# Kernel optimization log

Hardware: AMD Instinct MI355X
Metric: run time of the kernel (lower is better)

The kernel has to match this reference:

```python
import jax, jax.numpy as jnp
import numpy as np

B = 1024          # batch
D = 6             # data_dim
H = 128           # hidden_dim
VW = 256          # vf_hidden_dim (MLP width and output)
LS = 22           # logsig_dim (first entry dropped in vector field)
NI = 64           # number of log-signature intervals
NSTEPS = 64       # fixed Heun steps over [0, 1]


def setup_inputs() -> dict:
    key = jax.random.key(0)
    ks = jax.random.split(key, 12)
    ts = jnp.linspace(0.0, 1.0, NI + 1, dtype=jnp.float32)
    logsig = 0.1 * jax.random.normal(ks[0], (B, NI, LS), dtype=jnp.float32)
    x0 = jax.random.normal(ks[1], (B, D), dtype=jnp.float32)
    def lin(k, out_d, in_d):
        s = 1.0 / np.sqrt(in_d)
        kw, kb = jax.random.split(k)
        W = jax.random.uniform(kw, (out_d, in_d), jnp.float32, -s, s)
        b = jax.random.uniform(kb, (out_d,), jnp.float32, -s, s)
        return W, b
    W_vf1, b_vf1 = lin(ks[2], VW, H)    # VectorField MLP: hidden -> width
    W_vf2, b_vf2 = lin(ks[3], VW, VW)   # width -> vf out, final tanh
    Wm, bm = lin(ks[4], H * (LS - 1), VW)  # mlp_linear
    W1, b1 = lin(ks[5], H, D)           # linear1
    W2, b2 = lin(ks[6], 10, H)          # linear2 (label_dim=10)
    return {"ts": ts, "logsig": logsig, "x0": x0,
            "W_vf1": W_vf1, "b_vf1": b_vf1, "W_vf2": W_vf2, "b_vf2": b_vf2,
            "Wm": Wm, "bm": bm, "W1": W1, "b1": b1, "W2": W2, "b2": b2}


def reference(ts, logsig, x0, W_vf1, b_vf1, W_vf2, b_vf2, Wm, bm, W1, b1, W2, b2):
    intervals = ts                      # breakpoints, shape (NI+1,)
    dt = (ts[-1] - ts[0]) / NSTEPS
    ls_tail = logsig[:, :, 1:]          # (B, NI, LS-1), drop leading logsig term

    def vf(y):                          # VectorField MLP, batched: (B,H)->(B,VW)
        h = jax.nn.relu(jnp.einsum("bh,wh->bw", y, W_vf1) + b_vf1)
        return jnp.tanh(jnp.einsum("bw,vw->bv", h, W_vf2) + b_vf2)

    def func(t, y):                     # dy/dt, shape (B, H)
        idx = jnp.clip(jnp.searchsorted(intervals, t), 1, NI)
        A = (jnp.einsum("bv,ov->bo", vf(y), Wm) + bm).reshape(-1, H, LS - 1)
        ls = ls_tail[:, idx - 1]        # (B, LS-1)
        width = intervals[idx] - intervals[idx - 1]
        return jnp.einsum("bhl,bl->bh", A, ls) / width

    def heun_step(y, t):
        k1 = func(t, y)
        k2 = func(t + dt, y + dt * k1)
        return y + 0.5 * dt * (k1 + k2), None

    y0 = jnp.einsum("bd,hd->bh", x0, W1) + b1
    step_ts = ts[0] + dt * jnp.arange(NSTEPS, dtype=jnp.float32)
    yT, _ = jax.lax.scan(heun_step, y0, step_ts)
    return jax.nn.softmax(jnp.einsum("bh,ch->bc", yT, W2) + b2, axis=-1)
```

## Files before the change

### kernel.cpp

```cpp
#include <hip/hip_runtime.h>
#include <hip/hip_bf16.h>

typedef float f32x4 __attribute__((ext_vector_type(4)));
typedef int   i32x4 __attribute__((ext_vector_type(4)));
typedef short s16x8 __attribute__((ext_vector_type(8)));
typedef unsigned short u16;

#define NGP 32
#define BT 16
#define NWG 256
#define NTH 512
#define PREPTH 256
#define H 128
#define VW 256
#define NI 64
#define NSTEPS 64

#define OFF_FRAG16 0
#define OFF_WMQ    196608
#define OFF_BMF    884736
#define OFF_SCF    895488
#define OFF_SINV   896000
#define OFF_YBUF   896512
#define YBUF_BYTES 1048576

#define MFMA_BF16(a,b,c) __builtin_amdgcn_mfma_f32_16x16x32_bf16(a,b,c,0,0,0)
#define MFMA_I8(a,b,c)   __builtin_amdgcn_mfma_i32_16x16x64_i8(a,b,c,0,0,0)

__device__ __forceinline__ u16 bf16u(float f) {
  union { float f; unsigned u; } x; x.f = f;
  return (u16)((x.u + 0x7fffu + ((x.u >> 16) & 1u)) >> 16);
}
__device__ __forceinline__ float b2f(u16 u) {
  union { unsigned u; float f; } x; x.u = ((unsigned)u) << 16;
  return x.f;
}

__global__ void prep_scales(const float* __restrict__ Wm, char* __restrict__ ws) {
  __shared__ float red[4];
  const int tid = threadIdx.x;
  const int h = blockIdx.x;
  float m = 0.f;
  for (int i = tid; i < 21 * VW; i += PREPTH) m = fmaxf(m, fabsf(Wm[h * 21 * VW + i]));
  for (int off = 32; off > 0; off >>= 1) m = fmaxf(m, __shfl_down(m, off));
  if ((tid & 63) == 0) red[tid >> 6] = m;
  __syncthreads();
  if (tid == 0) {
    m = fmaxf(fmaxf(red[0], red[1]), fmaxf(red[2], red[3]));
    m = fmaxf(m, 1e-20f);
    ((float*)(ws + OFF_SCF))[h]  = m / 16129.f;
    ((float*)(ws + OFF_SINV))[h] = 127.f / m;
  }
}

__global__ void prep_pack(const float* __restrict__ Wvf1, const float* __restrict__ Wvf2,
                          const float* __restrict__ Wm, const float* __restrict__ bmv,
                          char* __restrict__ ws) {
  int idx = blockIdx.x * blockDim.x + threadIdx.x;
  if (idx < 98304) {
    u16* w16 = (u16*)(ws + OFF_FRAG16);
    float val;
    if (idx < 32768) {
      int e = idx;
      int j = e & 7, ln = (e >> 3) & 63, nt = (e >> 9) & 15, kk = e >> 13;
      val = Wvf1[(nt * 16 + (ln & 15)) * H + kk * 32 + (ln >> 4) * 8 + j];
    } else {
      int e = idx - 32768;
      int j = e & 7, ln = (e >> 3) & 63, nt = (e >> 9) & 15, kk = e >> 13;
      val = Wvf2[(nt * 16 + (ln & 15)) * VW + kk * 32 + (ln >> 4) * 8 + j];
    }
    w16[idx] = bf16u(val);
  } else if (idx < 98304 + 688128) {
    int b = idx - 98304;
    int j = b & 15, lane = (b >> 4) & 63, kk = (b >> 10) & 3, rem = b >> 12;
    int l = rem % 21, nt = rem / 21;
    int h = nt * 16 + (lane & 15);
    int w = kk * 64 + (lane >> 4) * 16 + j;
    float sinv = ((const float*)(ws + OFF_SINV))[h];
    float val = Wm[(size_t)(h * 21 + l) * VW + w];
    int q = (int)lrintf(val * sinv);
    q = min(127, max(-127, q));
    ((signed char*)(ws + OFF_WMQ))[b] = (signed char)q;
  } else if (idx < 98304 + 688128 + 2688) {
    int b = idx - (98304 + 688128);
    int hh = b & 15, rem = b >> 4;
    int l = rem % 21, nt = rem / 21;
    ((float*)(ws + OFF_BMF))[b] = bmv[(nt * 16 + hh) * 21 + l];
  }
}

__global__ __launch_bounds__(NTH, 1) void rde_main(
    const float* __restrict__ logsig, const float* __restrict__ x0,
    const float* __restrict__ W1, const float* __restrict__ b1,
    const float* __restrict__ bvf1, const float* __restrict__ bvf2,
    const float* __restrict__ W2, const float* __restrict__ b2,
    char* __restrict__ ws, float* __restrict__ out) {
  __shared__ __align__(16) signed char WmL[86016];
  __shared__ __align__(16) u16   YB [2][BT][H + 8];
  __shared__ __align__(16) u16   V1R[BT][VW + 8];
  __shared__ __align__(16) signed char V2QH[4096];
  __shared__ __align__(16) float LSF[2][2][21][BT];
  __shared__ __align__(16) float part[8][BT][17];
  __shared__ __align__(16) float bmL[336];
  __shared__ float scL[16];
  __shared__ float LG[32][10];

  const int tid = threadIdx.x;
  const int lane = tid & 63;
  const int wv = tid >> 6;
  const int c = lane & 15;
  const int kg = lane >> 4;
  const int bid = blockIdx.x;
  const int Gp = (bid & 7) * 4 + (bid >> 6);
  const int t = (bid >> 3) & 7;
  const int b0 = Gp * 32;
  unsigned* __restrict__ ybuf = (unsigned*)(ws + OFF_YBUF);
  const s16x8* __restrict__ fr16 = (const s16x8*)(ws + OFF_FRAG16);
  const f32x4 zf = {0.f, 0.f, 0.f, 0.f};
  const i32x4 zi = {0, 0, 0, 0};

  s16x8 w1r[2][4], w2r[2][8];
#pragma unroll
  for (int n = 0; n < 2; ++n) {
#pragma unroll
    for (int kk = 0; kk < 4; ++kk) w1r[n][kk] = fr16[(kk * 16 + wv * 2 + n) * 64 + lane];
#pragma unroll
    for (int kk = 0; kk < 8; ++kk) w2r[n][kk] = fr16[4096 + (kk * 16 + wv * 2 + n) * 64 + lane];
  }
  float bv1[2], bv2[2];
#pragma unroll
  for (int n = 0; n < 2; ++n) {
    bv1[n] = bvf1[wv * 32 + n * 16 + c];
    bv2[n] = bvf2[wv * 32 + n * 16 + c];
  }

  {
    const i32x4* wsrc = (const i32x4*)(ws + OFF_WMQ + t * 86016);
    i32x4* wdst = (i32x4*)WmL;
    for (int e = tid; e < 5376; e += NTH) wdst[e] = wsrc[e];
  }
  if (tid < 16) scL[tid] = ((const float*)(ws + OFF_SCF))[t * 16 + tid];
  for (int e = tid; e < 336; e += NTH) bmL[e] = ((const float*)(ws + OFF_BMF))[t * 336 + e];

  for (int e = tid; e < 2 * BT * H; e += NTH) {
    int tt = e >> 11, r = (e >> 7) & 15, h = e & 127;
    float a = b1[h];
#pragma unroll
    for (int d = 0; d < 6; ++d) a += x0[(b0 + tt * 16 + r) * 6 + d] * W1[h * 6 + d];
    YB[tt][r][h] = bf16u(a);
  }
  float y0s = 0.f, y1s = 0.f, yp0s = 0.f, yp1s = 0.f;
  if (tid < 256) {
    int r = tid >> 4, hh = tid & 15, h = t * 16 + hh;
    float a0 = b1[h], a1 = b1[h];
#pragma unroll
    for (int d = 0; d < 6; ++d) {
      a0 += x0[(b0 + r) * 6 + d] * W1[h * 6 + d];
      a1 += x0[(b0 + 16 + r) * 6 + d] * W1[h * 6 + d];
    }
    y0s = a0; y1s = a1;
  }

  auto STAGE = [&](int T, int iv) {
    for (int e = tid; e < BT * 21; e += NTH) {
      int r = e / 21, l = e - r * 21;
      LSF[T][iv & 1][l][r] = logsig[((size_t)(b0 + T * 16 + r) * NI + iv) * 22 + 1 + l];
    }
  };
  auto S1 = [&](int T) {
    s16x8 ay0 = *(const s16x8*)&YB[T][c][0 * 32 + kg * 8];
    s16x8 ay1 = *(const s16x8*)&YB[T][c][1 * 32 + kg * 8];
    s16x8 ay2 = *(const s16x8*)&YB[T][c][2 * 32 + kg * 8];
    s16x8 ay3 = *(const s16x8*)&YB[T][c][3 * 32 + kg * 8];
    f32x4 pA = MFMA_BF16(ay0, w1r[0][0], zf), pB = MFMA_BF16(ay0, w1r[1][0], zf);
    pA = MFMA_BF16(ay1, w1r[0][1], pA);  pB = MFMA_BF16(ay1, w1r[1][1], pB);
    pA = MFMA_BF16(ay2, w1r[0][2], pA);  pB = MFMA_BF16(ay2, w1r[1][2], pB);
    pA = MFMA_BF16(ay3, w1r[0][3], pA);  pB = MFMA_BF16(ay3, w1r[1][3], pB);
#pragma unroll
    for (int q = 0; q < 4; ++q) {
      V1R[kg * 4 + q][wv * 32 + c]      = bf16u(fmaxf(pA[q] + bv1[0], 0.f));
      V1R[kg * 4 + q][wv * 32 + 16 + c] = bf16u(fmaxf(pB[q] + bv1[1], 0.f));
    }
  };
  auto S2 = [&]() {
    s16x8 av0 = *(const s16x8*)&V1R[c][0 * 32 + kg * 8];
    s16x8 av1 = *(const s16x8*)&V1R[c][1 * 32 + kg * 8];
    s16x8 av2 = *(const s16x8*)&V1R[c][2 * 32 + kg * 8];
    s16x8 av3 = *(const s16x8*)&V1R[c][3 * 32 + kg * 8];
    s16x8 av4 = *(const s16x8*)&V1R[c][4 * 32 + kg * 8];
    s16x8 av5 = *(const s16x8*)&V1R[c][5 * 32 + kg * 8];
    s16x8 av6 = *(const s16x8*)&V1R[c][6 * 32 + kg * 8];
    s16x8 av7 = *(const s16x8*)&V1R[c][7 * 32 + kg * 8];
    f32x4 pA = MFMA_BF16(av0, w2r[0][0], zf), pB = MFMA_BF16(av0, w2r[1][0], zf);
    pA = MFMA_BF16(av1, w2r[0][1], pA);  pB = MFMA_BF16(av1, w2r[1][1], pB);
    pA = MFMA_BF16(av2, w2r[0][2], pA);  pB = MFMA_BF16(av2, w2r[1][2], pB);
    pA = MFMA_BF16(av3, w2r[0][3], pA);  pB = MFMA_BF16(av3, w2r[1][3], pB);
    pA = MFMA_BF16(av4, w2r[0][4], pA);  pB = MFMA_BF16(av4, w2r[1][4], pB);
    pA = MFMA_BF16(av5, w2r[0][5], pA);  pB = MFMA_BF16(av5, w2r[1][5], pB);
    pA = MFMA_BF16(av6, w2r[0][6], pA);  pB = MFMA_BF16(av6, w2r[1][6], pB);
    pA = MFMA_BF16(av7, w2r[0][7], pA);  pB = MFMA_BF16(av7, w2r[1][7], pB);
#pragma unroll
    for (int n = 0; n < 2; ++n) {
      f32x4 p = n ? pB : pA;
#pragma unroll
      for (int q = 0; q < 4; ++q) {
        float x = p[q] + bv2[n];
        float e2 = __expf(2.f * x);
        float t127 = fmaf(-254.f, __builtin_amdgcn_rcpf(e2 + 1.f), 127.f);
        int bo = ((wv >> 1) * 64 + ((wv & 1) * 2 + n) * 16 + kg * 4 + q) * 16 + c;
        V2QH[bo] = (signed char)(int)rintf(t127);
      }
    }
  };
  auto S3 = [&](int T, int lsb_) {
    i32x4 aih0 = *(const i32x4*)&V2QH[(0 * 64 + lane) * 16];
    i32x4 aih1 = *(const i32x4*)&V2QH[(1 * 64 + lane) * 16];
    i32x4 aih2 = *(const i32x4*)&V2QH[(2 * 64 + lane) * 16];
    i32x4 aih3 = *(const i32x4*)&V2QH[(3 * 64 + lane) * 16];
    const int nl = (wv < 5) ? 3 : 2;
    const int lb = (wv < 5) ? 3 * wv : 15 + 2 * (wv - 5);
    f32x4 acc = zf;
    for (int li = 0; li < nl; ++li) {
      int l = lb + li;
      const i32x4* bp = (const i32x4*)WmL + l * 256 + lane;
      i32x4 bq0 = bp[0], bq1 = bp[64], bq2 = bp[128], bq3 = bp[192];
      i32x4 PH = MFMA_I8(aih0, bq0, zi);
      PH = MFMA_I8(aih1, bq1, PH);
      PH = MFMA_I8(aih2, bq2, PH);
      PH = MFMA_I8(aih3, bq3, PH);
      f32x4 ls4 = *(const f32x4*)&LSF[T][lsb_][l][kg * 4];
#pragma unroll
      for (int q = 0; q < 4; ++q) acc[q] += ls4[q] * (float)PH[q];
    }
#pragma unroll
    for (int q = 0; q < 4; ++q) part[wv][kg * 4 + q][c] = acc[q];
  };
  auto S4 = [&](int T, int j, int lsb_, float& y, float& yp) {
    if (tid < 256) {
      int r = tid >> 4, hh = tid & 15;
      float s = ((part[0][r][hh] + part[1][r][hh]) + (part[2][r][hh] + part[3][r][hh])) +
                ((part[4][r][hh] + part[5][r][hh]) + (part[6][r][hh] + part[7][r][hh]));
      float bmd = 0.f;
#pragma unroll
      for (int l = 0; l < 21; ++l) bmd += LSF[T][lsb_][l][r] * bmL[l * 16 + hh];
      float raw = scL[hh] * s + bmd;
      float yn;
      if (!(j & 1)) { yp = y + 0.5f * raw; yn = y + raw; }
      else          { y = yp + 0.5f * raw; yn = y; }
      unsigned v = ((unsigned)(j + 1) << 16) | (unsigned)bf16u(yn);
      __hip_atomic_store(&ybuf[((Gp * 2 + T) * 2 + (j & 1)) * 2048 + r * 128 + t * 16 + hh],
                         v, __ATOMIC_RELAXED, __HIP_MEMORY_SCOPE_AGENT);
    }
  };
  auto S5 = [&](int T, int j) {
    const unsigned tg = (unsigned)(j + 1);
    const unsigned* pb = ybuf + ((Gp * 2 + T) * 2 + (j & 1)) * 2048;
    unsigned v0, v1, v2, v3;
#pragma unroll 1
    for (int sp = 0; sp < 60000; ++sp) {
      v0 = __hip_atomic_load(&pb[tid],        __ATOMIC_RELAXED, __HIP_MEMORY_SCOPE_AGENT);
      v1 = __hip_atomic_load(&pb[tid + 512],  __ATOMIC_RELAXED, __HIP_MEMORY_SCOPE_AGENT);
      v2 = __hip_atomic_load(&pb[tid + 1024], __ATOMIC_RELAXED, __HIP_MEMORY_SCOPE_AGENT);
      v3 = __hip_atomic_load(&pb[tid + 1536], __ATOMIC_RELAXED, __HIP_MEMORY_SCOPE_AGENT);
      unsigned mn = min(min(v0 >> 16, v1 >> 16), min(v2 >> 16, v3 >> 16));
      if (mn == tg) break;
    }
    YB[T][tid >> 7][tid & 127] = (u16)(v0 & 0xffffu);
    YB[T][(tid + 512) >> 7][(tid + 512) & 127] = (u16)(v1 & 0xffffu);
    YB[T][(tid + 1024) >> 7][(tid + 1024) & 127] = (u16)(v2 & 0xffffu);
    YB[T][(tid + 1536) >> 7][(tid + 1536) & 127] = (u16)(v3 & 0xffffu);
  };

  __syncthreads();

  STAGE(1, 0);
  __syncthreads();
  S1(1);
  __syncthreads();
  S2();
  __syncthreads();

#pragma unroll 1
  for (int j = 0; j < 2 * NSTEPS; ++j) {
    const int step_ = j >> 1, sub_ = j & 1;
    const int lsb_ = (sub_ ? step_ : (step_ > 0 ? step_ - 1 : 0)) & 1;
    if (!sub_) STAGE(0, step_);
    S1(0);
    S3(1, lsb_);
    __syncthreads();
    S4(1, j, lsb_, y1s, yp1s);
    S2();
    S5(1, j);
    __syncthreads();
    S3(0, lsb_);
    if (j < 2 * NSTEPS - 1) {
      if (sub_) STAGE(1, (j + 1) >> 1);
      S1(1);
    }
    __syncthreads();
    S4(0, j, lsb_, y0s, yp0s);
    if (j < 2 * NSTEPS - 1) S2();
    S5(0, j);
    __syncthreads();
  }

  if (t == 0) {
    for (int e = tid; e < 32 * 10; e += NTH) {
      int rr = e / 10, cc = e - rr * 10;
      float a = b2[cc];
#pragma unroll 4
      for (int h = 0; h < H; ++h) a += b2f(YB[rr >> 4][rr & 15][h]) * W2[cc * H + h];
      LG[rr][cc] = a;
    }
    __syncthreads();
    if (tid < 32) {
      float mx = -1e30f;
#pragma unroll
      for (int cc = 0; cc < 10; ++cc) mx = fmaxf(mx, LG[tid][cc]);
      float ex[10]; float s = 0.f;
#pragma unroll
      for (int cc = 0; cc < 10; ++cc) { ex[cc] = expf(LG[tid][cc] - mx); s += ex[cc]; }
      float inv = 1.f / s;
#pragma unroll
      for (int cc = 0; cc < 10; ++cc) out[(b0 + tid) * 10 + cc] = ex[cc] * inv;
    }
  }
}

extern "C" void kernel_launch(void* const* d_in, const int* in_sizes, int n_in,
                              void* d_out, int out_size, void* d_ws, size_t ws_size,
                              hipStream_t stream) {
  (void)in_sizes; (void)n_in; (void)out_size; (void)ws_size;
  const float* logsig = (const float*)d_in[1];
  const float* x0     = (const float*)d_in[2];
  const float* Wvf1   = (const float*)d_in[3];
  const float* bvf1   = (const float*)d_in[4];
  const float* Wvf2   = (const float*)d_in[5];
  const float* bvf2   = (const float*)d_in[6];
  const float* Wm     = (const float*)d_in[7];
  const float* bmv    = (const float*)d_in[8];
  const float* W1     = (const float*)d_in[9];
  const float* b1     = (const float*)d_in[10];
  const float* W2     = (const float*)d_in[11];
  const float* b2     = (const float*)d_in[12];
  char* ws = (char*)d_ws;

  prep_scales<<<128, PREPTH, 0, stream>>>(Wm, ws);
  prep_pack<<<3083, PREPTH, 0, stream>>>(Wvf1, Wvf2, Wm, bmv, ws);
  hipMemsetAsync(ws + OFF_YBUF, 0, YBUF_BYTES, stream);
  rde_main<<<NWG, NTH, 0, stream>>>(logsig, x0, W1, b1, bvf1, bvf2, W2, b2, ws,
                                    (float*)d_out);
}
```

Baseline: 572.5 us.

## Double workgroup to 1024 threads, split MLP tiles per wave, cache bias term

Moves the persistent kernel from 8 to 16 waves per block. In the two vector-field GEMMs each wave now computes one 16-column tile instead of two, and the int8 Wm contraction is spread over 16 waves. The logsig·bm bias dot product is computed only when the interval changes (first and odd substeps) and reused on the next even substep. The cross-block poll now has each thread load two adjacent words and write them to shared memory as one packed store. The aim is to shorten the serial per-substep critical path, at the cost of more threads competing for registers and a 16-way partial-sum reduction.

```diff
diff --git a/kernel.cpp b/kernel.cpp
--- a/kernel.cpp
+++ b/kernel.cpp
@@ -9,7 +9,7 @@
 #define NGP 32
 #define BT 16
 #define NWG 256
-#define NTH 512
+#define NTH 1024
 #define PREPTH 256
 #define H 128
 #define VW 256
@@ -100,7 +100,7 @@
   __shared__ __align__(16) u16   V1R[BT][VW + 8];
   __shared__ __align__(16) signed char V2QH[4096];
   __shared__ __align__(16) float LSF[2][2][21][BT];
-  __shared__ __align__(16) float part[8][BT][17];
+  __shared__ __align__(16) float part[16][BT][17];
   __shared__ __align__(16) float bmL[336];
   __shared__ float scL[16];
   __shared__ float LG[32][10];
@@ -119,20 +119,13 @@
   const f32x4 zf = {0.f, 0.f, 0.f, 0.f};
   const i32x4 zi = {0, 0, 0, 0};
 
-  s16x8 w1r[2][4], w2r[2][8];
-#pragma unroll
-  for (int n = 0; n < 2; ++n) {
-#pragma unroll
-    for (int kk = 0; kk < 4; ++kk) w1r[n][kk] = fr16[(kk * 16 + wv * 2 + n) * 64 + lane];
-#pragma unroll
-    for (int kk = 0; kk < 8; ++kk) w2r[n][kk] = fr16[4096 + (kk * 16 + wv * 2 + n) * 64 + lane];
-  }
-  float bv1[2], bv2[2];
-#pragma unroll
-  for (int n = 0; n < 2; ++n) {
-    bv1[n] = bvf1[wv * 32 + n * 16 + c];
-    bv2[n] = bvf2[wv * 32 + n * 16 + c];
-  }
+  s16x8 w1r[4], w2r[8];
+#pragma unroll
+  for (int kk = 0; kk < 4; ++kk) w1r[kk] = fr16[(kk * 16 + wv) * 64 + lane];
+#pragma unroll
+  for (int kk = 0; kk < 8; ++kk) w2r[kk] = fr16[4096 + (kk * 16 + wv) * 64 + lane];
+  const float bv1 = bvf1[wv * 16 + c];
+  const float bv2 = bvf2[wv * 16 + c];
 
   {
     const i32x4* wsrc = (const i32x4*)(ws + OFF_WMQ + t * 86016);
@@ -140,7 +133,7 @@
     for (int e = tid; e < 5376; e += NTH) wdst[e] = wsrc[e];
   }
   if (tid < 16) scL[tid] = ((const float*)(ws + OFF_SCF))[t * 16 + tid];
-  for (int e = tid; e < 336; e += NTH) bmL[e] = ((const float*)(ws + OFF_BMF))[t * 336 + e];
+  if (tid < 336) bmL[tid] = ((const float*)(ws + OFF_BMF))[t * 336 + tid];
 
   for (int e = tid; e < 2 * BT * H; e += NTH) {
     int tt = e >> 11, r = (e >> 7) & 15, h = e & 127;
@@ -150,6 +143,7 @@
     YB[tt][r][h] = bf16u(a);
   }
   float y0s = 0.f, y1s = 0.f, yp0s = 0.f, yp1s = 0.f;
+  float bmd0 = 0.f, bmd1 = 0.f;
   if (tid < 256) {
     int r = tid >> 4, hh = tid & 15, h = t * 16 + hh;
     float a0 = b1[h], a1 = b1[h];
@@ -162,8 +156,8 @@
   }
 
   auto STAGE = [&](int T, int iv) {
-    for (int e = tid; e < BT * 21; e += NTH) {
-      int r = e / 21, l = e - r * 21;
+    if (tid < BT * 21) {
+      int r = tid / 21, l = tid - r * 21;
       LSF[T][iv & 1][l][r] = logsig[((size_t)(b0 + T * 16 + r) * NI + iv) * 22 + 1 + l];
     }
   };
@@ -172,44 +166,38 @@
     s16x8 ay1 = *(const s16x8*)&YB[T][c][1 * 32 + kg * 8];
     s16x8 ay2 = *(const s16x8*)&YB[T][c][2 * 32 + kg * 8];
     s16x8 ay3 = *(const s16x8*)&YB[T][c][3 * 32 + kg * 8];
-    f32x4 pA = MFMA_BF16(ay0, w1r[0][0], zf), pB = MFMA_BF16(ay0, w1r[1][0], zf);
-    pA = MFMA_BF16(ay1, w1r[0][1], pA);  pB = MFMA_BF16(ay1, w1r[1][1], pB);
-    pA = MFMA_BF16(ay2, w1r[0][2], pA);  pB = MFMA_BF16(ay2, w1r[1][2], pB);
-    pA = MFMA_BF16(ay3, w1r[0][3], pA);  pB = MFMA_BF16(ay3, w1r[1][3], pB);
-#pragma unroll
-    for (int q = 0; q < 4; ++q) {
-      V1R[kg * 4 + q][wv * 32 + c]      = bf16u(fmaxf(pA[q] + bv1[0], 0.f));
-      V1R[kg * 4 + q][wv * 32 + 16 + c] = bf16u(fmaxf(pB[q] + bv1[1], 0.f));
-    }
+    f32x4 p = MFMA_BF16(ay0, w1r[0], zf);
+    p = MFMA_BF16(ay1, w1r[1], p);
+    p = MFMA_BF16(ay2, w1r[2], p);
+    p = MFMA_BF16(ay3, w1r[3], p);
+#pragma unroll
+    for (int q = 0; q < 4; ++q)
+      V1R[kg * 4 + q][wv * 16 + c] = bf16u(fmaxf(p[q] + bv1, 0.f));
   };
   auto S2 = [&]() {
     s16x8 av0 = *(const s16x8*)&V1R[c][0 * 32 + kg * 8];
     s16x8 av1 = *(const s16x8*)&V1R[c][1 * 32 + kg * 8];
     s16x8 av2 = *(const s16x8*)&V1R[c][2 * 32 + kg * 8];
     s16x8 av3 = *(const s16x8*)&V1R[c][3 * 32 + kg * 8];
+    f32x4 pLo = MFMA_BF16(av0, w2r[0], zf);
+    pLo = MFMA_BF16(av1, w2r[1], pLo);
+    pLo = MFMA_BF16(av2, w2r[2], pLo);
+    pLo = MFMA_BF16(av3, w2r[3], pLo);
     s16x8 av4 = *(const s16x8*)&V1R[c][4 * 32 + kg * 8];
     s16x8 av5 = *(const s16x8*)&V1R[c][5 * 32 + kg * 8];
     s16x8 av6 = *(const s16x8*)&V1R[c][6 * 32 + kg * 8];
     s16x8 av7 = *(const s16x8*)&V1R[c][7 * 32 + kg * 8];
-    f32x4 pA = MFMA_BF16(av0, w2r[0][0], zf), pB = MFMA_BF16(av0, w2r[1][0], zf);
-    pA = MFMA_BF16(av1, w2r[0][1], pA);  pB = MFMA_BF16(av1, w2r[1][1], pB);
-    pA = MFMA_BF16(av2, w2r[0][2], pA);  pB = MFMA_BF16(av2, w2r[1][2], pB);
-    pA = MFMA_BF16(av3, w2r[0][3], pA);  pB = MFMA_BF16(av3, w2r[1][3], pB);
-    pA = MFMA_BF16(av4, w2r[0][4], pA);  pB = MFMA_BF16(av4, w2r[1][4], pB);
-    pA = MFMA_BF16(av5, w2r[0][5], pA);  pB = MFMA_BF16(av5, w2r[1][5], pB);
-    pA = MFMA_BF16(av6, w2r[0][6], pA);  pB = MFMA_BF16(av6, w2r[1][6], pB);
-    pA = MFMA_BF16(av7, w2r[0][7], pA);  pB = MFMA_BF16(av7, w2r[1][7], pB);
-#pragma unroll
-    for (int n = 0; n < 2; ++n) {
-      f32x4 p = n ? pB : pA;
-#pragma unroll
-      for (int q = 0; q < 4; ++q) {
-        float x = p[q] + bv2[n];
-        float e2 = __expf(2.f * x);
-        float t127 = fmaf(-254.f, __builtin_amdgcn_rcpf(e2 + 1.f), 127.f);
-        int bo = ((wv >> 1) * 64 + ((wv & 1) * 2 + n) * 16 + kg * 4 + q) * 16 + c;
-        V2QH[bo] = (signed char)(int)rintf(t127);
-      }
+    f32x4 pHi = MFMA_BF16(av4, w2r[4], zf);
+    pHi = MFMA_BF16(av5, w2r[5], pHi);
+    pHi = MFMA_BF16(av6, w2r[6], pHi);
+    pHi = MFMA_BF16(av7, w2r[7], pHi);
+#pragma unroll
+    for (int q = 0; q < 4; ++q) {
+      float x = pLo[q] + pHi[q] + bv2;
+      float e2 = __expf(2.f * x);
+      float t127 = fmaf(-254.f, __builtin_amdgcn_rcpf(e2 + 1.f), 127.f);
+      int bo = (((wv >> 2) * 64) + (wv & 3) * 16 + kg * 4 + q) * 16 + c;
+      V2QH[bo] = (signed char)(int)rintf(t127);
     }
   };
   auto S3 = [&](int T, int lsb_) {
@@ -217,58 +205,60 @@
     i32x4 aih1 = *(const i32x4*)&V2QH[(1 * 64 + lane) * 16];
     i32x4 aih2 = *(const i32x4*)&V2QH[(2 * 64 + lane) * 16];
     i32x4 aih3 = *(const i32x4*)&V2QH[(3 * 64 + lane) * 16];
-    const int nl = (wv < 5) ? 3 : 2;
-    const int lb = (wv < 5) ? 3 * wv : 15 + 2 * (wv - 5);
+    const int nl3 = (wv < 5) ? 2 : 1;
+    const int lb3 = (wv < 5) ? 2 * wv : 10 + (wv - 5);
     f32x4 acc = zf;
-    for (int li = 0; li < nl; ++li) {
-      int l = lb + li;
-      const i32x4* bp = (const i32x4*)WmL + l * 256 + lane;
-      i32x4 bq0 = bp[0], bq1 = bp[64], bq2 = bp[128], bq3 = bp[192];
-      i32x4 PH = MFMA_I8(aih0, bq0, zi);
-      PH = MFMA_I8(aih1, bq1, PH);
-      PH = MFMA_I8(aih2, bq2, PH);
-      PH = MFMA_I8(aih3, bq3, PH);
-      f32x4 ls4 = *(const f32x4*)&LSF[T][lsb_][l][kg * 4];
-#pragma unroll
-      for (int q = 0; q < 4; ++q) acc[q] += ls4[q] * (float)PH[q];
+#pragma unroll
+    for (int li = 0; li < 2; ++li) {
+      if (li < nl3) {
+        int l = lb3 + li;
+        const i32x4* bp = (const i32x4*)WmL + l * 256 + lane;
+        i32x4 bq0 = bp[0], bq1 = bp[64], bq2 = bp[128], bq3 = bp[192];
+        i32x4 PH = MFMA_I8(aih0, bq0, zi);
+        PH = MFMA_I8(aih1, bq1, PH);
+        PH = MFMA_I8(aih2, bq2, PH);
+        PH = MFMA_I8(aih3, bq3, PH);
+        f32x4 ls4 = *(const f32x4*)&LSF[T][lsb_][l][kg * 4];
+#pragma unroll
+        for (int q = 0; q < 4; ++q) acc[q] += ls4[q] * (float)PH[q];
+      }
     }
 #pragma unroll
     for (int q = 0; q < 4; ++q) part[wv][kg * 4 + q][c] = acc[q];
   };
-  auto S4 = [&](int T, int j, int lsb_, float& y, float& yp) {
+  auto S4 = [&](int T, int jj, int lsb_, float& y, float& yp, float& bmdc) {
     if (tid < 256) {
       int r = tid >> 4, hh = tid & 15;
-      float s = ((part[0][r][hh] + part[1][r][hh]) + (part[2][r][hh] + part[3][r][hh])) +
-                ((part[4][r][hh] + part[5][r][hh]) + (part[6][r][hh] + part[7][r][hh]));
-      float bmd = 0.f;
-#pragma unroll
-      for (int l = 0; l < 21; ++l) bmd += LSF[T][lsb_][l][r] * bmL[l * 16 + hh];
-      float raw = scL[hh] * s + bmd;
+      float s = 0.f;
+#pragma unroll
+      for (int w = 0; w < 16; ++w) s += part[w][r][hh];
+      if (jj == 0 || (jj & 1)) {
+        float bmd = 0.f;
+#pragma unroll
+        for (int l = 0; l < 21; ++l) bmd += LSF[T][lsb_][l][r] * bmL[l * 16 + hh];
+        bmdc = bmd;
+      }
+      float raw = scL[hh] * s + bmdc;
       float yn;
-      if (!(j & 1)) { yp = y + 0.5f * raw; yn = y + raw; }
-      else          { y = yp + 0.5f * raw; yn = y; }
-      unsigned v = ((unsigned)(j + 1) << 16) | (unsigned)bf16u(yn);
-      __hip_atomic_store(&ybuf[((Gp * 2 + T) * 2 + (j & 1)) * 2048 + r * 128 + t * 16 + hh],
+      if (!(jj & 1)) { yp = y + 0.5f * raw; yn = y + raw; }
+      else           { y = yp + 0.5f * raw; yn = y; }
+      unsigned v = ((unsigned)(jj + 1) << 16) | (unsigned)bf16u(yn);
+      __hip_atomic_store(&ybuf[((Gp * 2 + T) * 2 + (jj & 1)) * 2048 + r * 128 + t * 16 + hh],
                          v, __ATOMIC_RELAXED, __HIP_MEMORY_SCOPE_AGENT);
     }
   };
-  auto S5 = [&](int T, int j) {
-    const unsigned tg = (unsigned)(j + 1);
-    const unsigned* pb = ybuf + ((Gp * 2 + T) * 2 + (j & 1)) * 2048;
-    unsigned v0, v1, v2, v3;
+  auto S5 = [&](int T, int jj) {
+    const unsigned tg = (unsigned)(jj + 1);
+    const unsigned* pb = ybuf + ((Gp * 2 + T) * 2 + (jj & 1)) * 2048 + tid * 2;
+    unsigned v0, v1;
 #pragma unroll 1
     for (int sp = 0; sp < 60000; ++sp) {
-      v0 = __hip_atomic_load(&pb[tid],        __ATOMIC_RELAXED, __HIP_MEMORY_SCOPE_AGENT);
-      v1 = __hip_atomic_load(&pb[tid + 512],  __ATOMIC_RELAXED, __HIP_MEMORY_SCOPE_AGENT);
-      v2 = __hip_atomic_load(&pb[tid + 1024], __ATOMIC_RELAXED, __HIP_MEMORY_SCOPE_AGENT);
-      v3 = __hip_atomic_load(&pb[tid + 1536], __ATOMIC_RELAXED, __HIP_MEMORY_SCOPE_AGENT);
-      unsigned mn = min(min(v0 >> 16, v1 >> 16), min(v2 >> 16, v3 >> 16));
-      if (mn == tg) break;
-    }
-    YB[T][tid >> 7][tid & 127] = (u16)(v0 & 0xffffu);
-    YB[T][(tid + 512) >> 7][(tid + 512) & 127] = (u16)(v1 & 0xffffu);
-    YB[T][(tid + 1024) >> 7][(tid + 1024) & 127] = (u16)(v2 & 0xffffu);
-    YB[T][(tid + 1536) >> 7][(tid + 1536) & 127] = (u16)(v3 & 0xffffu);
+      v0 = __hip_atomic_load(pb,     __ATOMIC_RELAXED, __HIP_MEMORY_SCOPE_AGENT);
+      v1 = __hip_atomic_load(pb + 1, __ATOMIC_RELAXED, __HIP_MEMORY_SCOPE_AGENT);
+      if (min(v0 >> 16, v1 >> 16) == tg) break;
+    }
+    int e0 = tid * 2, r = e0 >> 7, h0 = e0 & 127;
+    *(unsigned*)&YB[T][r][h0] = (v0 & 0xffffu) | (v1 << 16);
   };
 
   __syncthreads();
@@ -288,7 +278,7 @@
     S1(0);
     S3(1, lsb_);
     __syncthreads();
-    S4(1, j, lsb_, y1s, yp1s);
+    S4(1, j, lsb_, y1s, yp1s, bmd1);
     S2();
     S5(1, j);
     __syncthreads();
@@ -298,7 +288,7 @@
       S1(1);
     }
     __syncthreads();
-    S4(0, j, lsb_, y0s, yp0s);
+    S4(0, j, lsb_, y0s, yp0s, bmd0);
     if (j < 2 * NSTEPS - 1) S2();
     S5(0, j);
     __syncthreads();
```

Result: slower. 774.3 us (+35.2%).

## Swap MFMA operand order to pack intermediate activations and cache bias dot

Applied to the files above, without the earlier changes.

Swaps the A/B operands of the bf16 MFMAs so each lane owns 4 consecutive output rows, which lets the ReLU output and the int8 tanh output be written as packed 64-bit and 32-bit LDS stores in fragment-ready layout instead of scattered 16-bit and byte stores. The bias dot product over the logsig tail is computed only when the logsig interval changes and then reused. Bias vectors are loaded as float4, and the strided staging loops become single guarded assignments. The aim is fewer LDS store instructions and less per-substep ALU work on the serial critical path; correctness depends on the new fragment layout matching what S2 and S3 read.

```diff
diff --git a/kernel.cpp b/kernel.cpp
--- a/kernel.cpp
+++ b/kernel.cpp
@@ -97,7 +97,7 @@
     char* __restrict__ ws, float* __restrict__ out) {
   __shared__ __align__(16) signed char WmL[86016];
   __shared__ __align__(16) u16   YB [2][BT][H + 8];
-  __shared__ __align__(16) u16   V1R[BT][VW + 8];
+  __shared__ __align__(16) u16   V1F[4096];
   __shared__ __align__(16) signed char V2QH[4096];
   __shared__ __align__(16) float LSF[2][2][21][BT];
   __shared__ __align__(16) float part[8][BT][17];
@@ -127,11 +127,11 @@
 #pragma unroll
     for (int kk = 0; kk < 8; ++kk) w2r[n][kk] = fr16[4096 + (kk * 16 + wv * 2 + n) * 64 + lane];
   }
-  float bv1[2], bv2[2];
+  f32x4 bv1v[2], bv2v[2];
 #pragma unroll
   for (int n = 0; n < 2; ++n) {
-    bv1[n] = bvf1[wv * 32 + n * 16 + c];
-    bv2[n] = bvf2[wv * 32 + n * 16 + c];
+    bv1v[n] = *(const f32x4*)&bvf1[wv * 32 + n * 16 + kg * 4];
+    bv2v[n] = *(const f32x4*)&bvf2[wv * 32 + n * 16 + kg * 4];
   }
 
   {
@@ -140,7 +140,7 @@
     for (int e = tid; e < 5376; e += NTH) wdst[e] = wsrc[e];
   }
   if (tid < 16) scL[tid] = ((const float*)(ws + OFF_SCF))[t * 16 + tid];
-  for (int e = tid; e < 336; e += NTH) bmL[e] = ((const float*)(ws + OFF_BMF))[t * 336 + e];
+  if (tid < 336) bmL[tid] = ((const float*)(ws + OFF_BMF))[t * 336 + tid];
 
   for (int e = tid; e < 2 * BT * H; e += NTH) {
     int tt = e >> 11, r = (e >> 7) & 15, h = e & 127;
@@ -150,6 +150,7 @@
     YB[tt][r][h] = bf16u(a);
   }
   float y0s = 0.f, y1s = 0.f, yp0s = 0.f, yp1s = 0.f;
+  float bmd0 = 0.f, bmd1 = 0.f;
   if (tid < 256) {
     int r = tid >> 4, hh = tid & 15, h = t * 16 + hh;
     float a0 = b1[h], a1 = b1[h];
@@ -162,8 +163,8 @@
   }
 
   auto STAGE = [&](int T, int iv) {
-    for (int e = tid; e < BT * 21; e += NTH) {
-      int r = e / 21, l = e - r * 21;
+    if (tid < BT * 21) {
+      int r = tid / 21, l = tid - r * 21;
       LSF[T][iv & 1][l][r] = logsig[((size_t)(b0 + T * 16 + r) * NI + iv) * 22 + 1 + l];
     }
   };
@@ -172,44 +173,52 @@
     s16x8 ay1 = *(const s16x8*)&YB[T][c][1 * 32 + kg * 8];
     s16x8 ay2 = *(const s16x8*)&YB[T][c][2 * 32 + kg * 8];
     s16x8 ay3 = *(const s16x8*)&YB[T][c][3 * 32 + kg * 8];
-    f32x4 pA = MFMA_BF16(ay0, w1r[0][0], zf), pB = MFMA_BF16(ay0, w1r[1][0], zf);
-    pA = MFMA_BF16(ay1, w1r[0][1], pA);  pB = MFMA_BF16(ay1, w1r[1][1], pB);
-    pA = MFMA_BF16(ay2, w1r[0][2], pA);  pB = MFMA_BF16(ay2, w1r[1][2], pB);
-    pA = MFMA_BF16(ay3, w1r[0][3], pA);  pB = MFMA_BF16(ay3, w1r[1][3], pB);
-#pragma unroll
-    for (int q = 0; q < 4; ++q) {
-      V1R[kg * 4 + q][wv * 32 + c]      = bf16u(fmaxf(pA[q] + bv1[0], 0.f));
-      V1R[kg * 4 + q][wv * 32 + 16 + c] = bf16u(fmaxf(pB[q] + bv1[1], 0.f));
-    }
-  };
-  auto S2 = [&]() {
-    s16x8 av0 = *(const s16x8*)&V1R[c][0 * 32 + kg * 8];
-    s16x8 av1 = *(const s16x8*)&V1R[c][1 * 32 + kg * 8];
-    s16x8 av2 = *(const s16x8*)&V1R[c][2 * 32 + kg * 8];
-    s16x8 av3 = *(const s16x8*)&V1R[c][3 * 32 + kg * 8];
-    s16x8 av4 = *(const s16x8*)&V1R[c][4 * 32 + kg * 8];
-    s16x8 av5 = *(const s16x8*)&V1R[c][5 * 32 + kg * 8];
-    s16x8 av6 = *(const s16x8*)&V1R[c][6 * 32 + kg * 8];
-    s16x8 av7 = *(const s16x8*)&V1R[c][7 * 32 + kg * 8];
-    f32x4 pA = MFMA_BF16(av0, w2r[0][0], zf), pB = MFMA_BF16(av0, w2r[1][0], zf);
-    pA = MFMA_BF16(av1, w2r[0][1], pA);  pB = MFMA_BF16(av1, w2r[1][1], pB);
-    pA = MFMA_BF16(av2, w2r[0][2], pA);  pB = MFMA_BF16(av2, w2r[1][2], pB);
-    pA = MFMA_BF16(av3, w2r[0][3], pA);  pB = MFMA_BF16(av3, w2r[1][3], pB);
-    pA = MFMA_BF16(av4, w2r[0][4], pA);  pB = MFMA_BF16(av4, w2r[1][4], pB);
-    pA = MFMA_BF16(av5, w2r[0][5], pA);  pB = MFMA_BF16(av5, w2r[1][5], pB);
-    pA = MFMA_BF16(av6, w2r[0][6], pA);  pB = MFMA_BF16(av6, w2r[1][6], pB);
-    pA = MFMA_BF16(av7, w2r[0][7], pA);  pB = MFMA_BF16(av7, w2r[1][7], pB);
+    f32x4 pA = MFMA_BF16(w1r[0][0], ay0, zf), pB = MFMA_BF16(w1r[1][0], ay0, zf);
+    pA = MFMA_BF16(w1r[0][1], ay1, pA);  pB = MFMA_BF16(w1r[1][1], ay1, pB);
+    pA = MFMA_BF16(w1r[0][2], ay2, pA);  pB = MFMA_BF16(w1r[1][2], ay2, pB);
+    pA = MFMA_BF16(w1r[0][3], ay3, pA);  pB = MFMA_BF16(w1r[1][3], ay3, pB);
 #pragma unroll
     for (int n = 0; n < 2; ++n) {
       f32x4 p = n ? pB : pA;
+      unsigned lo = (unsigned)bf16u(fmaxf(p[0] + bv1v[n][0], 0.f)) |
+                    ((unsigned)bf16u(fmaxf(p[1] + bv1v[n][1], 0.f)) << 16);
+      unsigned hi = (unsigned)bf16u(fmaxf(p[2] + bv1v[n][2], 0.f)) |
+                    ((unsigned)bf16u(fmaxf(p[3] + bv1v[n][3], 0.f)) << 16);
+      int u64i = ((wv * 4 + n * 2 + (kg >> 1)) * 16 + c) * 2 + (kg & 1);
+      ((unsigned long long*)V1F)[u64i] =
+          (unsigned long long)lo | ((unsigned long long)hi << 32);
+    }
+  };
+  auto S2 = [&]() {
+    const s16x8* v1f8 = (const s16x8*)V1F;
+    s16x8 av0 = v1f8[(0 * 4 + kg) * 16 + c];
+    s16x8 av1 = v1f8[(1 * 4 + kg) * 16 + c];
+    s16x8 av2 = v1f8[(2 * 4 + kg) * 16 + c];
+    s16x8 av3 = v1f8[(3 * 4 + kg) * 16 + c];
+    s16x8 av4 = v1f8[(4 * 4 + kg) * 16 + c];
+    s16x8 av5 = v1f8[(5 * 4 + kg) * 16 + c];
+    s16x8 av6 = v1f8[(6 * 4 + kg) * 16 + c];
+    s16x8 av7 = v1f8[(7 * 4 + kg) * 16 + c];
+    f32x4 pA = MFMA_BF16(w2r[0][0], av0, zf), pB = MFMA_BF16(w2r[1][0], av0, zf);
+    pA = MFMA_BF16(w2r[0][1], av1, pA);  pB = MFMA_BF16(w2r[1][1], av1, pB);
+    pA = MFMA_BF16(w2r[0][2], av2, pA);  pB = MFMA_BF16(w2r[1][2], av2, pB);
+    pA = MFMA_BF16(w2r[0][3], av3, pA);  pB = MFMA_BF16(w2r[1][3], av3, pB);
+    pA = MFMA_BF16(w2r[0][4], av4, pA);  pB = MFMA_BF16(w2r[1][4], av4, pB);
+    pA = MFMA_BF16(w2r[0][5], av5, pA);  pB = MFMA_BF16(w2r[1][5], av5, pB);
+    pA = MFMA_BF16(w2r[0][6], av6, pA);  pB = MFMA_BF16(w2r[1][6], av6, pB);
+    pA = MFMA_BF16(w2r[0][7], av7, pA);  pB = MFMA_BF16(w2r[1][7], av7, pB);
+#pragma unroll
+    for (int n = 0; n < 2; ++n) {
+      f32x4 p = n ? pB : pA;
+      unsigned wq = 0;
 #pragma unroll
       for (int q = 0; q < 4; ++q) {
-        float x = p[q] + bv2[n];
+        float x = p[q] + bv2v[n][q];
         float e2 = __expf(2.f * x);
         float t127 = fmaf(-254.f, __builtin_amdgcn_rcpf(e2 + 1.f), 127.f);
-        int bo = ((wv >> 1) * 64 + ((wv & 1) * 2 + n) * 16 + kg * 4 + q) * 16 + c;
-        V2QH[bo] = (signed char)(int)rintf(t127);
+        wq |= ((unsigned)((int)rintf(t127) & 255)) << (q * 8);
       }
+      ((unsigned*)V2QH)[((2 * wv + n) * 16 + c) * 4 + kg] = wq;
     }
   };
   auto S3 = [&](int T, int lsb_) {
@@ -235,26 +244,29 @@
 #pragma unroll
     for (int q = 0; q < 4; ++q) part[wv][kg * 4 + q][c] = acc[q];
   };
-  auto S4 = [&](int T, int j, int lsb_, float& y, float& yp) {
+  auto S4 = [&](int T, int jj, int lsb_, float& y, float& yp, float& bmdc) {
     if (tid < 256) {
       int r = tid >> 4, hh = tid & 15;
       float s = ((part[0][r][hh] + part[1][r][hh]) + (part[2][r][hh] + part[3][r][hh])) +
                 ((part[4][r][hh] + part[5][r][hh]) + (part[6][r][hh] + part[7][r][hh]));
-      float bmd = 0.f;
-#pragma unroll
-      for (int l = 0; l < 21; ++l) bmd += LSF[T][lsb_][l][r] * bmL[l * 16 + hh];
-      float raw = scL[hh] * s + bmd;
+      if (jj == 0 || (jj & 1)) {
+        float bmd = 0.f;
+#pragma unroll
+        for (int l = 0; l < 21; ++l) bmd += LSF[T][lsb_][l][r] * bmL[l * 16 + hh];
+        bmdc = bmd;
+      }
+      float raw = scL[hh] * s + bmdc;
       float yn;
-      if (!(j & 1)) { yp = y + 0.5f * raw; yn = y + raw; }
-      else          { y = yp + 0.5f * raw; yn = y; }
-      unsigned v = ((unsigned)(j + 1) << 16) | (unsigned)bf16u(yn);
-      __hip_atomic_store(&ybuf[((Gp * 2 + T) * 2 + (j & 1)) * 2048 + r * 128 + t * 16 + hh],
+      if (!(jj & 1)) { yp = y + 0.5f * raw; yn = y + raw; }
+      else           { y = yp + 0.5f * raw; yn = y; }
+      unsigned v = ((unsigned)(jj + 1) << 16) | (unsigned)bf16u(yn);
+      __hip_atomic_store(&ybuf[((Gp * 2 + T) * 2 + (jj & 1)) * 2048 + r * 128 + t * 16 + hh],
                          v, __ATOMIC_RELAXED, __HIP_MEMORY_SCOPE_AGENT);
     }
   };
-  auto S5 = [&](int T, int j) {
-    const unsigned tg = (unsigned)(j + 1);
-    const unsigned* pb = ybuf + ((Gp * 2 + T) * 2 + (j & 1)) * 2048;
+  auto S5 = [&](int T, int jj) {
+    const unsigned tg = (unsigned)(jj + 1);
+    const unsigned* pb = ybuf + ((Gp * 2 + T) * 2 + (jj & 1)) * 2048;
     unsigned v0, v1, v2, v3;
 #pragma unroll 1
     for (int sp = 0; sp < 60000; ++sp) {
@@ -288,7 +300,7 @@
     S1(0);
     S3(1, lsb_);
     __syncthreads();
-    S4(1, j, lsb_, y1s, yp1s);
+    S4(1, j, lsb_, y1s, yp1s, bmd1);
     S2();
     S5(1, j);
     __syncthreads();
@@ -298,7 +310,7 @@
       S1(1);
     }
     __syncthreads();
-    S4(0, j, lsb_, y0s, yp0s);
+    S4(0, j, lsb_, y0s, yp0s, bmd0);
     if (j < 2 * NSTEPS - 1) S2();
     S5(0, j);
     __syncthreads();
```

After: 600.0 us. 1.05x slower.

## Process four 16-row batch tiles per workgroup, halving the grid to 128 workgroups

Applied to the files above, without the earlier changes.

Each workgroup now owns 64 batch rows (four 16-row tiles) instead of 32. The grid shrinks from 256 to 128 workgroups, and the V1R, V2QH and part scratch buffers are double-buffered so two tiles move through each pipeline stage between barriers. The cross-workgroup y exchange polls two tiles per wait. The aim is to amortise the per-substep barriers and global spin-wait latency over more work, at the cost of using half as many CUs and doing more serial work per workgroup.

```diff
diff --git a/kernel.cpp b/kernel.cpp
--- a/kernel.cpp
+++ b/kernel.cpp
@@ -6,9 +6,8 @@
 typedef short s16x8 __attribute__((ext_vector_type(8)));
 typedef unsigned short u16;
 
-#define NGP 32
 #define BT 16
-#define NWG 256
+#define NWG 128
 #define NTH 512
 #define PREPTH 256
 #define H 128
@@ -96,14 +95,13 @@
     const float* __restrict__ W2, const float* __restrict__ b2,
     char* __restrict__ ws, float* __restrict__ out) {
   __shared__ __align__(16) signed char WmL[86016];
-  __shared__ __align__(16) u16   YB [2][BT][H + 8];
-  __shared__ __align__(16) u16   V1R[BT][VW + 8];
-  __shared__ __align__(16) signed char V2QH[4096];
-  __shared__ __align__(16) float LSF[2][2][21][BT];
-  __shared__ __align__(16) float part[8][BT][17];
+  __shared__ __align__(16) u16   YB [4][BT][H + 8];
+  __shared__ __align__(16) u16   V1R[2][BT][VW + 8];
+  __shared__ __align__(16) signed char V2QH[2][4096];
+  __shared__ __align__(16) float LSF[4][2][21][BT];
+  __shared__ __align__(16) float part[2][8][BT][17];
   __shared__ __align__(16) float bmL[336];
   __shared__ float scL[16];
-  __shared__ float LG[32][10];
 
   const int tid = threadIdx.x;
   const int lane = tid & 63;
@@ -111,9 +109,9 @@
   const int c = lane & 15;
   const int kg = lane >> 4;
   const int bid = blockIdx.x;
-  const int Gp = (bid & 7) * 4 + (bid >> 6);
-  const int t = (bid >> 3) & 7;
-  const int b0 = Gp * 32;
+  const int Gp = bid & 15;
+  const int t = bid >> 4;
+  const int b0 = Gp * 64;
   unsigned* __restrict__ ybuf = (unsigned*)(ws + OFF_YBUF);
   const s16x8* __restrict__ fr16 = (const s16x8*)(ws + OFF_FRAG16);
   const f32x4 zf = {0.f, 0.f, 0.f, 0.f};
@@ -140,34 +138,38 @@
     for (int e = tid; e < 5376; e += NTH) wdst[e] = wsrc[e];
   }
   if (tid < 16) scL[tid] = ((const float*)(ws + OFF_SCF))[t * 16 + tid];
-  for (int e = tid; e < 336; e += NTH) bmL[e] = ((const float*)(ws + OFF_BMF))[t * 336 + e];
-
-  for (int e = tid; e < 2 * BT * H; e += NTH) {
+  if (tid < 336) bmL[tid] = ((const float*)(ws + OFF_BMF))[t * 336 + tid];
+
+  for (int e = tid; e < 4 * BT * H; e += NTH) {
     int tt = e >> 11, r = (e >> 7) & 15, h = e & 127;
     float a = b1[h];
 #pragma unroll
     for (int d = 0; d < 6; ++d) a += x0[(b0 + tt * 16 + r) * 6 + d] * W1[h * 6 + d];
     YB[tt][r][h] = bf16u(a);
   }
-  float y0s = 0.f, y1s = 0.f, yp0s = 0.f, yp1s = 0.f;
+  float y0s = 0.f, y1s = 0.f, y2s = 0.f, y3s = 0.f;
+  float yp0s = 0.f, yp1s = 0.f, yp2s = 0.f, yp3s = 0.f;
   if (tid < 256) {
     int r = tid >> 4, hh = tid & 15, h = t * 16 + hh;
-    float a0 = b1[h], a1 = b1[h];
+    float a0 = b1[h], a1 = b1[h], a2 = b1[h], a3 = b1[h];
 #pragma unroll
     for (int d = 0; d < 6; ++d) {
-      a0 += x0[(b0 + r) * 6 + d] * W1[h * 6 + d];
-      a1 += x0[(b0 + 16 + r) * 6 + d] * W1[h * 6 + d];
-    }
-    y0s = a0; y1s = a1;
+      float w = W1[h * 6 + d];
+      a0 += x0[(b0 + r) * 6 + d] * w;
+      a1 += x0[(b0 + 16 + r) * 6 + d] * w;
+      a2 += x0[(b0 + 32 + r) * 6 + d] * w;
+      a3 += x0[(b0 + 48 + r) * 6 + d] * w;
+    }
+    y0s = a0; y1s = a1; y2s = a2; y3s = a3;
   }
 
   auto STAGE = [&](int T, int iv) {
-    for (int e = tid; e < BT * 21; e += NTH) {
-      int r = e / 21, l = e - r * 21;
+    if (tid < BT * 21) {
+      int r = tid / 21, l = tid - r * 21;
       LSF[T][iv & 1][l][r] = logsig[((size_t)(b0 + T * 16 + r) * NI + iv) * 22 + 1 + l];
     }
   };
-  auto S1 = [&](int T) {
+  auto S1 = [&](int T, int p) {
     s16x8 ay0 = *(const s16x8*)&YB[T][c][0 * 32 + kg * 8];
     s16x8 ay1 = *(const s16x8*)&YB[T][c][1 * 32 + kg * 8];
     s16x8 ay2 = *(const s16x8*)&YB[T][c][2 * 32 + kg * 8];
@@ -178,19 +180,19 @@
     pA = MFMA_BF16(ay3, w1r[0][3], pA);  pB = MFMA_BF16(ay3, w1r[1][3], pB);
 #pragma unroll
     for (int q = 0; q < 4; ++q) {
-      V1R[kg * 4 + q][wv * 32 + c]      = bf16u(fmaxf(pA[q] + bv1[0], 0.f));
-      V1R[kg * 4 + q][wv * 32 + 16 + c] = bf16u(fmaxf(pB[q] + bv1[1], 0.f));
-    }
-  };
-  auto S2 = [&]() {
-    s16x8 av0 = *(const s16x8*)&V1R[c][0 * 32 + kg * 8];
-    s16x8 av1 = *(const s16x8*)&V1R[c][1 * 32 + kg * 8];
-    s16x8 av2 = *(const s16x8*)&V1R[c][2 * 32 + kg * 8];
-    s16x8 av3 = *(const s16x8*)&V1R[c][3 * 32 + kg * 8];
-    s16x8 av4 = *(const s16x8*)&V1R[c][4 * 32 + kg * 8];
-    s16x8 av5 = *(const s16x8*)&V1R[c][5 * 32 + kg * 8];
-    s16x8 av6 = *(const s16x8*)&V1R[c][6 * 32 + kg * 8];
-    s16x8 av7 = *(const s16x8*)&V1R[c][7 * 32 + kg * 8];
+      V1R[p][kg * 4 + q][wv * 32 + c]      = bf16u(fmaxf(pA[q] + bv1[0], 0.f));
+      V1R[p][kg * 4 + q][wv * 32 + 16 + c] = bf16u(fmaxf(pB[q] + bv1[1], 0.f));
+    }
+  };
+  auto S2 = [&](int p) {
+    s16x8 av0 = *(const s16x8*)&V1R[p][c][0 * 32 + kg * 8];
+    s16x8 av1 = *(const s16x8*)&V1R[p][c][1 * 32 + kg * 8];
+    s16x8 av2 = *(const s16x8*)&V1R[p][c][2 * 32 + kg * 8];
+    s16x8 av3 = *(const s16x8*)&V1R[p][c][3 * 32 + kg * 8];
+    s16x8 av4 = *(const s16x8*)&V1R[p][c][4 * 32 + kg * 8];
+    s16x8 av5 = *(const s16x8*)&V1R[p][c][5 * 32 + kg * 8];
+    s16x8 av6 = *(const s16x8*)&V1R[p][c][6 * 32 + kg * 8];
+    s16x8 av7 = *(const s16x8*)&V1R[p][c][7 * 32 + kg * 8];
     f32x4 pA = MFMA_BF16(av0, w2r[0][0], zf), pB = MFMA_BF16(av0, w2r[1][0], zf);
     pA = MFMA_BF16(av1, w2r[0][1], pA);  pB = MFMA_BF16(av1, w2r[1][1], pB);
     pA = MFMA_BF16(av2, w2r[0][2], pA);  pB = MFMA_BF16(av2, w2r[1][2], pB);
@@ -201,22 +203,22 @@
     pA = MFMA_BF16(av7, w2r[0][7], pA);  pB = MFMA_BF16(av7, w2r[1][7], pB);
 #pragma unroll
     for (int n = 0; n < 2; ++n) {
-      f32x4 p = n ? pB : pA;
+      f32x4 pp = n ? pB : pA;
 #pragma unroll
       for (int q = 0; q < 4; ++q) {
-        float x = p[q] + bv2[n];
+        float x = pp[q] + bv2[n];
         float e2 = __expf(2.f * x);
         float t127 = fmaf(-254.f, __builtin_amdgcn_rcpf(e2 + 1.f), 127.f);
         int bo = ((wv >> 1) * 64 + ((wv & 1) * 2 + n) * 16 + kg * 4 + q) * 16 + c;
-        V2QH[bo] = (signed char)(int)rintf(t127);
+        V2QH[p][bo] = (signed char)(int)rintf(t127);
       }
     }
   };
-  auto S3 = [&](int T, int lsb_) {
-    i32x4 aih0 = *(const i32x4*)&V2QH[(0 * 64 + lane) * 16];
-    i32x4 aih1 = *(const i32x4*)&V2QH[(1 * 64 + lane) * 16];
-    i32x4 aih2 = *(const i32x4*)&V2QH[(2 * 64 + lane) * 16];
-    i32x4 aih3 = *(const i32x4*)&V2QH[(3 * 64 + lane) * 16];
+  auto S3 = [&](int T, int p, int lsb_) {
+    i32x4 aih0 = *(const i32x4*)&V2QH[p][(0 * 64 + lane) * 16];
+    i32x4 aih1 = *(const i32x4*)&V2QH[p][(1 * 64 + lane) * 16];
+    i32x4 aih2 = *(const i32x4*)&V2QH[p][(2 * 64 + lane) * 16];
+    i32x4 aih3 = *(const i32x4*)&V2QH[p][(3 * 64 + lane) * 16];
     const int nl = (wv < 5) ? 3 : 2;
     const int lb = (wv < 5) ? 3 * wv : 15 + 2 * (wv - 5);
     f32x4 acc = zf;
@@ -233,13 +235,15 @@
       for (int q = 0; q < 4; ++q) acc[q] += ls4[q] * (float)PH[q];
     }
 #pragma unroll
-    for (int q = 0; q < 4; ++q) part[wv][kg * 4 + q][c] = acc[q];
-  };
-  auto S4 = [&](int T, int j, int lsb_, float& y, float& yp) {
+    for (int q = 0; q < 4; ++q) part[p][wv][kg * 4 + q][c] = acc[q];
+  };
+  auto S4 = [&](int T, int p, int j, int lsb_, float& y, float& yp) {
     if (tid < 256) {
       int r = tid >> 4, hh = tid & 15;
-      float s = ((part[0][r][hh] + part[1][r][hh]) + (part[2][r][hh] + part[3][r][hh])) +
-                ((part[4][r][hh] + part[5][r][hh]) + (part[6][r][hh] + part[7][r][hh]));
+      float s = ((part[p][0][r][hh] + part[p][1][r][hh]) +
+                 (part[p][2][r][hh] + part[p][3][r][hh])) +
+                ((part[p][4][r][hh] + part[p][5][r][hh]) +
+                 (part[p][6][r][hh] + part[p][7][r][hh]));
       float bmd = 0.f;
 #pragma unroll
       for (int l = 0; l < 21; ++l) bmd += LSF[T][lsb_][l][r] * bmL[l * 16 + hh];
@@ -248,78 +252,99 @@
       if (!(j & 1)) { yp = y + 0.5f * raw; yn = y + raw; }
       else          { y = yp + 0.5f * raw; yn = y; }
       unsigned v = ((unsigned)(j + 1) << 16) | (unsigned)bf16u(yn);
-      __hip_atomic_store(&ybuf[((Gp * 2 + T) * 2 + (j & 1)) * 2048 + r * 128 + t * 16 + hh],
+      __hip_atomic_store(&ybuf[((Gp * 4 + T) * 2 + (j & 1)) * 2048 + r * 128 + t * 16 + hh],
                          v, __ATOMIC_RELAXED, __HIP_MEMORY_SCOPE_AGENT);
     }
   };
-  auto S5 = [&](int T, int j) {
+  auto S5_2 = [&](int Ta, int Tb, int j) {
     const unsigned tg = (unsigned)(j + 1);
-    const unsigned* pb = ybuf + ((Gp * 2 + T) * 2 + (j & 1)) * 2048;
-    unsigned v0, v1, v2, v3;
+    const unsigned* pa = ybuf + ((Gp * 4 + Ta) * 2 + (j & 1)) * 2048;
+    const unsigned* pb = ybuf + ((Gp * 4 + Tb) * 2 + (j & 1)) * 2048;
+    unsigned a0, a1, a2, a3, e0, e1, e2, e3;
 #pragma unroll 1
     for (int sp = 0; sp < 60000; ++sp) {
-      v0 = __hip_atomic_load(&pb[tid],        __ATOMIC_RELAXED, __HIP_MEMORY_SCOPE_AGENT);
-      v1 = __hip_atomic_load(&pb[tid + 512],  __ATOMIC_RELAXED, __HIP_MEMORY_SCOPE_AGENT);
-      v2 = __hip_atomic_load(&pb[tid + 1024], __ATOMIC_RELAXED, __HIP_MEMORY_SCOPE_AGENT);
-      v3 = __hip_atomic_load(&pb[tid + 1536], __ATOMIC_RELAXED, __HIP_MEMORY_SCOPE_AGENT);
-      unsigned mn = min(min(v0 >> 16, v1 >> 16), min(v2 >> 16, v3 >> 16));
+      a0 = __hip_atomic_load(&pa[tid],        __ATOMIC_RELAXED, __HIP_MEMORY_SCOPE_AGENT);
+      a1 = __hip_atomic_load(&pa[tid + 512],  __ATOMIC_RELAXED, __HIP_MEMORY_SCOPE_AGENT);
+      a2 = __hip_atomic_load(&pa[tid + 1024], __ATOMIC_RELAXED, __HIP_MEMORY_SCOPE_AGENT);
+      a3 = __hip_atomic_load(&pa[tid + 1536], __ATOMIC_RELAXED, __HIP_MEMORY_SCOPE_AGENT);
+      e0 = __hip_atomic_load(&pb[tid],        __ATOMIC_RELAXED, __HIP_MEMORY_SCOPE_AGENT);
+      e1 = __hip_atomic_load(&pb[tid + 512],  __ATOMIC_RELAXED, __HIP_MEMORY_SCOPE_AGENT);
+      e2 = __hip_atomic_load(&pb[tid + 1024], __ATOMIC_RELAXED, __HIP_MEMORY_SCOPE_AGENT);
+      e3 = __hip_atomic_load(&pb[tid + 1536], __ATOMIC_RELAXED, __HIP_MEMORY_SCOPE_AGENT);
+      unsigned mn = min(min(a0 >> 16, a1 >> 16), min(a2 >> 16, a3 >> 16));
+      mn = min(mn, min(min(e0 >> 16, e1 >> 16), min(e2 >> 16, e3 >> 16)));
       if (mn == tg) break;
     }
-    YB[T][tid >> 7][tid & 127] = (u16)(v0 & 0xffffu);
-    YB[T][(tid + 512) >> 7][(tid + 512) & 127] = (u16)(v1 & 0xffffu);
-    YB[T][(tid + 1024) >> 7][(tid + 1024) & 127] = (u16)(v2 & 0xffffu);
-    YB[T][(tid + 1536) >> 7][(tid + 1536) & 127] = (u16)(v3 & 0xffffu);
+    YB[Ta][tid >> 7][tid & 127] = (u16)(a0 & 0xffffu);
+    YB[Ta][(tid + 512) >> 7][(tid + 512) & 127] = (u16)(a1 & 0xffffu);
+    YB[Ta][(tid + 1024) >> 7][(tid + 1024) & 127] = (u16)(a2 & 0xffffu);
+    YB[Ta][(tid + 1536) >> 7][(tid + 1536) & 127] = (u16)(a3 & 0xffffu);
+    YB[Tb][tid >> 7][tid & 127] = (u16)(e0 & 0xffffu);
+    YB[Tb][(tid + 512) >> 7][(tid + 512) & 127] = (u16)(e1 & 0xffffu);
+    YB[Tb][(tid + 1024) >> 7][(tid + 1024) & 127] = (u16)(e2 & 0xffffu);
+    YB[Tb][(tid + 1536) >> 7][(tid + 1536) & 127] = (u16)(e3 & 0xffffu);
   };
 
   __syncthreads();
 
   STAGE(1, 0);
-  __syncthreads();
-  S1(1);
-  __syncthreads();
-  S2();
+  STAGE(3, 0);
+  __syncthreads();
+  S1(1, 0);
+  S1(3, 1);
+  __syncthreads();
+  S2(0);
+  S2(1);
   __syncthreads();
 
 #pragma unroll 1
   for (int j = 0; j < 2 * NSTEPS; ++j) {
     const int step_ = j >> 1, sub_ = j & 1;
     const int lsb_ = (sub_ ? step_ : (step_ > 0 ? step_ - 1 : 0)) & 1;
-    if (!sub_) STAGE(0, step_);
-    S1(0);
-    S3(1, lsb_);
-    __syncthreads();
-    S4(1, j, lsb_, y1s, yp1s);
-    S2();
-    S5(1, j);
-    __syncthreads();
-    S3(0, lsb_);
+    if (!sub_) { STAGE(0, step_); STAGE(2, step_); }
+    S1(0, 0);
+    S1(2, 1);
+    S3(1, 0, lsb_);
+    S3(3, 1, lsb_);
+    __syncthreads();
+    S4(1, 0, j, lsb_, y1s, yp1s);
+    S4(3, 1, j, lsb_, y3s, yp3s);
+    S2(0);
+    S2(1);
+    S5_2(1, 3, j);
+    __syncthreads();
+    S3(0, 0, lsb_);
+    S3(2, 1, lsb_);
     if (j < 2 * NSTEPS - 1) {
-      if (sub_) STAGE(1, (j + 1) >> 1);
-      S1(1);
-    }
-    __syncthreads();
-    S4(0, j, lsb_, y0s, yp0s);
-    if (j < 2 * NSTEPS - 1) S2();
-    S5(0, j);
-    __syncthreads();
-  }
-
+      if (sub_) { STAGE(1, (j + 1) >> 1); STAGE(3, (j + 1) >> 1); }
+      S1(1, 0);
+      S1(3, 1);
+    }
+    __syncthreads();
+    S4(0, 0, j, lsb_, y0s, yp0s);
+    S4(2, 1, j, lsb_, y2s, yp2s);
+    if (j < 2 * NSTEPS - 1) { S2(0); S2(1); }
+    S5_2(0, 2, j);
+    __syncthreads();
+  }
+
+  float* LG = (float*)part;
   if (t == 0) {
-    for (int e = tid; e < 32 * 10; e += NTH) {
+    for (int e = tid; e < 64 * 10; e += NTH) {
       int rr = e / 10, cc = e - rr * 10;
       float a = b2[cc];
 #pragma unroll 4
       for (int h = 0; h < H; ++h) a += b2f(YB[rr >> 4][rr & 15][h]) * W2[cc * H + h];
-      LG[rr][cc] = a;
-    }
-    __syncthreads();
-    if (tid < 32) {
+      LG[rr * 10 + cc] = a;
+    }
+    __syncthreads();
+    if (tid < 64) {
       float mx = -1e30f;
 #pragma unroll
-      for (int cc = 0; cc < 10; ++cc) mx = fmaxf(mx, LG[tid][cc]);
+      for (int cc = 0; cc < 10; ++cc) mx = fmaxf(mx, LG[tid * 10 + cc]);
       float ex[10]; float s = 0.f;
 #pragma unroll
-      for (int cc = 0; cc < 10; ++cc) { ex[cc] = expf(LG[tid][cc] - mx); s += ex[cc]; }
+      for (int cc = 0; cc < 10; ++cc) { ex[cc] = expf(LG[tid * 10 + cc] - mx); s += ex[cc]; }
       float inv = 1.f / s;
 #pragma unroll
       for (int cc = 0; cc < 10; ++cc) out[(b0 + tid) * 10 + cc] = ex[cc] * inv;
```

Result: slower. 932.6 us (+62.9%).
